# Performance work log

Hardware: AMD Instinct MI355X
Metric: run time of the kernel (lower is better)

## Reference

```python
import jax, jax.numpy as jnp
import numpy as np

B = 32768                 # batch size (number of variants)
NUM_READ_FEATURES = 11
NUM_INFO_FEATURES = 9
PHI_DIMS = [NUM_READ_FEATURES, 64, 64]
OMEGA_DIMS = [NUM_INFO_FEATURES, 64, 64]
RHO_DIMS = [2 * 64 + 64, 128, 64, 1]
CAL_DIMS = [2, 5, 5, 1]


def _counts():
    # deterministic ragged group sizes in [5, 32], mean ~18.5, all nonempty
    return 5 + (np.arange(2 * B) % 28)


def _mlp_params(key, dims, prefix, out):
    for i, (din, dout) in enumerate(zip(dims[:-1], dims[1:])):
        key, k = jax.random.split(key)
        out[f"{prefix}_w{i}"] = (jax.random.normal(k, (din, dout), jnp.float32)
                                  / np.sqrt(din).astype(np.float32))
        out[f"{prefix}_b{i}"] = jnp.zeros((dout,), jnp.float32)
    return key


def _mlp(x, ws_bs):
    # Linear -> ReLU between layers, no activation after the last layer
    n = len(ws_bs) // 2
    for i in range(n):
        x = x @ ws_bs[2 * i] + ws_bs[2 * i + 1]
        if i < n - 1:
            x = jax.nn.relu(x)
    return x


def setup_inputs() -> dict:
    key = jax.random.key(0)
    counts = _counts()
    n_reads = int(counts.sum())  # 1,212,320
    key, k1, k2 = jax.random.split(key, 3)
    out = {
        "reads": jax.random.normal(k1, (n_reads, NUM_READ_FEATURES), jnp.float32),
        "info": jax.random.normal(k2, (B, NUM_INFO_FEATURES), jnp.float32),
        "end_indices": jnp.asarray(np.cumsum(counts), dtype=jnp.int64),
    }
    key = _mlp_params(key, PHI_DIMS, "phi", out)
    key = _mlp_params(key, OMEGA_DIMS, "omega", out)
    key = _mlp_params(key, RHO_DIMS, "rho", out)
    key = _mlp_params(key, CAL_DIMS, "cal", out)
    out["max_logit"] = jnp.asarray(10.0, jnp.float32)
    return out


def reference(reads, info, end_indices,
              phi_w0, phi_b0, phi_w1, phi_b1,
              omega_w0, omega_b0, omega_w1, omega_b1,
              rho_w0, rho_b0, rho_w1, rho_b1, rho_w2, rho_b2,
              cal_w0, cal_b0, cal_w1, cal_b1, cal_w2, cal_b2,
              max_logit):
    n_reads = reads.shape[0]
    num_seg = 2 * B
    # read r belongs to segment j where end_indices[j-1] <= r < end_indices[j]
    seg_ids = jnp.searchsorted(end_indices, jnp.arange(n_reads), side="right")

    phi_reads = jax.nn.sigmoid(_mlp(reads, [phi_w0, phi_b0, phi_w1, phi_b1]))  # [N, 64]
    weights = jnp.ones((n_reads, 1), phi_reads.dtype)  # weight_range == 0
    weighted = weights * phi_reads

    read_sums = jax.ops.segment_sum(weighted, seg_ids, num_segments=num_seg)      # [2B, 64]
    weight_sums = jax.ops.segment_sum(weights, seg_ids, num_segments=num_seg)     # [2B, 1]
    read_means = read_sums / weight_sums
    sq_weight_sums = jax.ops.segment_sum(jnp.square(weights), seg_ids, num_segments=num_seg)
    eff_counts = jnp.square(weight_sums) / sq_weight_sums                          # [2B, 1]

    ref_means, alt_means = read_means[:B], read_means[B:]
    eff_ref, eff_alt = eff_counts[:B], eff_counts[B:]

    omega_info = jax.nn.sigmoid(_mlp(info, [omega_w0, omega_b0, omega_w1, omega_b1]))
    concatenated = jnp.concatenate([ref_means, alt_means, omega_info], axis=1)     # [B, 192]
    logits = jnp.squeeze(_mlp(concatenated, [rho_w0, rho_b0, rho_w1, rho_b1, rho_w2, rho_b2]), -1)

    # Calibration: temperature from sqrt(alt_count), sqrt(ref_count)
    sqrt_counts = jnp.concatenate([jnp.sqrt(eff_alt), jnp.sqrt(eff_ref)], axis=1)  # [B, 2]
    temperatures = jnp.squeeze(_mlp(sqrt_counts, [cal_w0, cal_b0, cal_w1, cal_b1, cal_w2, cal_b2]), -1)
    calibrated = logits * temperatures
    return max_logit * jnp.tanh(calibrated / max_logit)
```

## Files before the change

### kernel.cpp

```cpp
#include <hip/hip_runtime.h>
#include <hip/hip_bf16.h>
#include <math.h>

#define NB 32768
#define NSEG 65536
#define NRF 11
#define NIF 9

typedef __attribute__((ext_vector_type(8))) short bf16x8;
typedef __attribute__((ext_vector_type(4))) float f32x4;

__device__ __forceinline__ short to_bf(float f) {
    __hip_bfloat16 h = __float2bfloat16(f);
    return *reinterpret_cast<short*>(&h);
}
__device__ __forceinline__ float bf2f(short s) {
    __hip_bfloat16 h = *reinterpret_cast<__hip_bfloat16*>(&s);
    return __bfloat162float(h);
}

__global__ __launch_bounds__(256) void k0_prep(
    const float* __restrict__ rw0, const float* __restrict__ rw1,
    const float* __restrict__ pw0, const float* __restrict__ pw1,
    short* __restrict__ w0th, short* __restrict__ w0tl,
    short* __restrict__ w1th, short* __restrict__ w1tl,
    short* __restrict__ p_w0t, short* __restrict__ p_w1t)
{
    const int idx = blockIdx.x * 256 + threadIdx.x;
    if (idx < 192 * 128) {
        const int k = idx >> 7, col = idx & 127;
        const float v = rw0[idx];
        const short hi = to_bf(v);
        const short lo = to_bf(v - bf2f(hi));
        w0th[col * 192 + k] = hi;
        w0tl[col * 192 + k] = lo;
    }
    if (idx < 128 * 64) {
        const int k = idx >> 6, col = idx & 63;
        const float v = rw1[idx];
        const short hi = to_bf(v);
        const short lo = to_bf(v - bf2f(hi));
        w1th[col * 128 + k] = hi;
        w1tl[col * 128 + k] = lo;
    }
    if (idx < 64 * 16) {
        const int col = idx >> 4, k = idx & 15;
        p_w0t[idx] = (k < NRF) ? to_bf(pw0[k * 64 + col]) : (short)0;
    }
    if (idx < 64 * 64) {
        const int col = idx >> 6, k = idx & 63;
        p_w1t[idx] = to_bf(pw1[k * 64 + col]);
    }
}

__global__ __launch_bounds__(256, 4) void k1_phi_mfma3(
    const float* __restrict__ reads,
    const int* __restrict__ endi,
    const short* __restrict__ p_w0t, const short* __restrict__ p_w1t,
    const float* __restrict__ b0, const float* __restrict__ b1,
    float* __restrict__ means)
{
    __shared__ short XA[256][24];
    __shared__ short HB[4][16][64];
    __shared__ int   smeta[9];

    const int tid  = threadIdx.x;
    const int lane = tid & 63;
    const int w    = tid >> 6;
    const int lg   = lane >> 4;
    const int lr   = lane & 15;
    const int k0   = lg * 8;
    const int s0   = blockIdx.x * 8;

    if (tid < 9) {
        const int s = s0 + tid - 1;
        smeta[tid] = (s < 0) ? 0 : endi[s];
    }
    __syncthreads();
    const int rb    = smeta[0];
    const int nrows = smeta[8] - rb;

    const int total = nrows * NRF;
    const float* __restrict__ rbase = reads + (size_t)rb * NRF;
    for (int i = tid; i < total; i += 256) {
        const int row = i / NRF;
        const int col = i - row * NRF;
        XA[row][col] = to_bf(rbase[i]);
    }
    for (int r = tid; r < nrows; r += 256) {
        XA[r][11] = 0;
        *(short4*)&XA[r][12] = (short4){0, 0, 0, 0};
    }
    __syncthreads();

    bf16x8 aW0[4];
#pragma unroll
    for (int nt = 0; nt < 4; ++nt) {
        bf16x8 z = {0, 0, 0, 0, 0, 0, 0, 0};
        if (lg < 2) z = *(const bf16x8*)&p_w0t[(nt * 16 + lr) * 16 + k0];
        aW0[nt] = z;
    }
    bf16x8 bW1[4][2];
#pragma unroll
    for (int nt = 0; nt < 4; ++nt)
#pragma unroll
        for (int ks = 0; ks < 2; ++ks)
            bW1[nt][ks] = *(const bf16x8*)&p_w1t[(nt * 16 + lr) * 64 + ks * 32 + k0];

    f32x4 cbias0[4];
#pragma unroll
    for (int nt = 0; nt < 4; ++nt)
#pragma unroll
        for (int q = 0; q < 4; ++q) cbias0[nt][q] = b0[nt * 16 + 4 * lg + q];
    f32x4 cbias1[4];
#pragma unroll
    for (int nt = 0; nt < 4; ++nt) {
        const float bv = b1[nt * 16 + lr];
#pragma unroll
        for (int q = 0; q < 4; ++q) cbias1[nt][q] = bv;
    }

    for (int q = 0; q < 2; ++q) {
        const int ls  = q * 4 + w;
        const int st  = smeta[ls] - rb;
        const int cnt = smeta[ls + 1] - smeta[ls];
        const int ntl = (cnt + 15) >> 4;
        float segsum[4] = {0.f, 0.f, 0.f, 0.f};

        for (int tt = 0; tt < ntl; ++tt) {
            int lrow = st + tt * 16 + lr;
            lrow = (lrow < nrows) ? lrow : (nrows - 1);
            bf16x8 xb = {0, 0, 0, 0, 0, 0, 0, 0};
            if (lg < 2) xb = *(const bf16x8*)&XA[lrow][k0];

            f32x4 d[4];
#pragma unroll
            for (int nt = 0; nt < 4; ++nt)
                d[nt] = __builtin_amdgcn_mfma_f32_16x16x32_bf16(aW0[nt], xb, cbias0[nt], 0, 0, 0);

#pragma unroll
            for (int nt = 0; nt < 4; ++nt) {
                short4 hp;
                hp.x = to_bf(fmaxf(d[nt][0], 0.f));
                hp.y = to_bf(fmaxf(d[nt][1], 0.f));
                hp.z = to_bf(fmaxf(d[nt][2], 0.f));
                hp.w = to_bf(fmaxf(d[nt][3], 0.f));
                const int blk = (2 * nt + (lg >> 1) + lr) & 7;
                *(short4*)&HB[w][lr][(blk << 3) + ((lg & 1) << 2)] = hp;
            }
            const bf16x8 h0 = *(const bf16x8*)&HB[w][lr][(((lg + lr) & 7) << 3)];
            const bf16x8 h1 = *(const bf16x8*)&HB[w][lr][(((4 + lg + lr) & 7) << 3)];
            f32x4 o[4];
#pragma unroll
            for (int nt = 0; nt < 4; ++nt) {
                f32x4 t = __builtin_amdgcn_mfma_f32_16x16x32_bf16(h0, bW1[nt][0], cbias1[nt], 0, 0, 0);
                o[nt]   = __builtin_amdgcn_mfma_f32_16x16x32_bf16(h1, bW1[nt][1], t, 0, 0, 0);
            }
            const int rowg = tt * 16 + 4 * lg;
#pragma unroll
            for (int nt = 0; nt < 4; ++nt) {
                float s = 0.f;
#pragma unroll
                for (int q2 = 0; q2 < 4; ++q2) {
                    const float p = __builtin_amdgcn_rcpf(1.f + __expf(-o[nt][q2]));
                    s += (rowg + q2 < cnt) ? p : 0.f;
                }
                s += __shfl_xor(s, 16);
                s += __shfl_xor(s, 32);
                segsum[nt] += s;
            }
        }
        if (lg == 0) {
            const float inv = 1.f / (float)cnt;
#pragma unroll
            for (int nt = 0; nt < 4; ++nt)
                means[(size_t)(s0 + ls) * 64 + nt * 16 + lr] = segsum[nt] * inv;
        }
    }
}

__global__ __launch_bounds__(256) void k2_omega(
    const float* __restrict__ info,
    const float* __restrict__ w0, const float* __restrict__ b0,
    const float* __restrict__ w1, const float* __restrict__ b1,
    float* __restrict__ om)
{
    __shared__ float hbuf[4][64];
    const int lane = threadIdx.x & 63;
    const int wid  = threadIdx.x >> 6;
    const int wg   = __builtin_amdgcn_readfirstlane((int)(blockIdx.x * 4 + wid));

    float w0c[NIF];
#pragma unroll
    for (int k = 0; k < NIF; ++k) w0c[k] = w0[k * 64 + lane];
    float w1c[64];
#pragma unroll
    for (int i = 0; i < 64; ++i) w1c[i] = w1[i * 64 + lane];
    const float b0l = b0[lane];
    const float b1l = b1[lane];

    for (int i = 0; i < 8; ++i) {
        const int b = wg * 8 + i;
        const float* __restrict__ x = info + (size_t)b * NIF;
        float h = b0l;
#pragma unroll
        for (int k = 0; k < NIF; ++k) h = fmaf(x[k], w0c[k], h);
        h = fmaxf(h, 0.f);
        hbuf[wid][lane] = h;
        float o = b1l;
        const float4* h4 = (const float4*)(&hbuf[wid][0]);
#pragma unroll
        for (int q = 0; q < 16; ++q) {
            float4 hv = h4[q];
            o = fmaf(hv.x, w1c[4 * q + 0], o);
            o = fmaf(hv.y, w1c[4 * q + 1], o);
            o = fmaf(hv.z, w1c[4 * q + 2], o);
            o = fmaf(hv.w, w1c[4 * q + 3], o);
        }
        om[(size_t)b * 64 + lane] = 1.f / (1.f + __expf(-o));
    }
}

__global__ __launch_bounds__(256) void k3_rho_mfma(
    const float* __restrict__ means, const float* __restrict__ om,
    const int* __restrict__ endi,
    const short* __restrict__ w0th, const short* __restrict__ w0tl,
    const short* __restrict__ w1th, const short* __restrict__ w1tl,
    const float* __restrict__ rb0, const float* __restrict__ rb1,
    const float* __restrict__ rw2, const float* __restrict__ rb2,
    const float* __restrict__ cw0, const float* __restrict__ cb0,
    const float* __restrict__ cw1, const float* __restrict__ cb1,
    const float* __restrict__ cw2, const float* __restrict__ cb2,
    const float* __restrict__ max_logit,
    float* __restrict__ out)
{
    __shared__ __align__(16) char smemA[18432];
    __shared__ __align__(16) char smemB[34816];
    short (*XH)[72]  = (short(*)[72])smemA;
    short (*XL)[72]  = (short(*)[72])(smemA + 9216);
    short (*HH)[136] = (short(*)[136])smemB;
    short (*HL)[136] = (short(*)[136])(smemB + 17408);
    float (*h2T)[68] = (float(*)[68])smemA;

    const int tid  = threadIdx.x;
    const int lane = tid & 63;
    const int w    = tid >> 6;
    const int lg   = lane >> 4;
    const int lr   = lane & 15;
    const int k0   = lg * 8;
    const int b0i  = blockIdx.x * 64;

    const int wbase = w * 32;
    float bias0[2];
#pragma unroll
    for (int nt = 0; nt < 2; ++nt) bias0[nt] = rb0[wbase + nt * 16 + lr];

    f32x4 acc[4][2];
#pragma unroll
    for (int rt = 0; rt < 4; ++rt)
#pragma unroll
        for (int nt = 0; nt < 2; ++nt) acc[rt][nt] = (f32x4){0.f, 0.f, 0.f, 0.f};

    for (int c = 0; c < 3; ++c) {
        const float* __restrict__ src =
            (c == 0) ? means + (size_t)b0i * 64 :
            (c == 1) ? means + (size_t)(NB + b0i) * 64 :
                       om    + (size_t)b0i * 64;
        __syncthreads();
        for (int idx = tid; idx < 64 * 64; idx += 256) {
            const int row = idx >> 6, col = idx & 63;
            const float v = src[(size_t)row * 64 + col];
            const short hi = to_bf(v);
            const short lo = to_bf(v - bf2f(hi));
            XH[row][col] = hi;
            XL[row][col] = lo;
        }
        __syncthreads();

#pragma unroll
        for (int ks = 0; ks < 2; ++ks) {
            const int koff = c * 64 + ks * 32 + k0;
            bf16x8 Bh[2], Bl[2];
#pragma unroll
            for (int nt = 0; nt < 2; ++nt) {
                const int col = wbase + nt * 16 + lr;
                Bh[nt] = *(const bf16x8*)&w0th[(size_t)col * 192 + koff];
                Bl[nt] = *(const bf16x8*)&w0tl[(size_t)col * 192 + koff];
            }
#pragma unroll
            for (int rt = 0; rt < 4; ++rt) {
                const bf16x8 Ah = *(const bf16x8*)&XH[rt * 16 + lr][ks * 32 + k0];
                const bf16x8 Al = *(const bf16x8*)&XL[rt * 16 + lr][ks * 32 + k0];
#pragma unroll
                for (int nt = 0; nt < 2; ++nt) {
                    acc[rt][nt] = __builtin_amdgcn_mfma_f32_16x16x32_bf16(Ah, Bh[nt], acc[rt][nt], 0, 0, 0);
                    acc[rt][nt] = __builtin_amdgcn_mfma_f32_16x16x32_bf16(Al, Bh[nt], acc[rt][nt], 0, 0, 0);
                    acc[rt][nt] = __builtin_amdgcn_mfma_f32_16x16x32_bf16(Ah, Bl[nt], acc[rt][nt], 0, 0, 0);
                }
            }
        }
    }
    __syncthreads();
#pragma unroll
    for (int rt = 0; rt < 4; ++rt)
#pragma unroll
        for (int nt = 0; nt < 2; ++nt)
#pragma unroll
            for (int r = 0; r < 4; ++r) {
                const int row = rt * 16 + 4 * lg + r;
                const int col = wbase + nt * 16 + lr;
                const float v = fmaxf(acc[rt][nt][r] + bias0[nt], 0.f);
                const short hi = to_bf(v);
                HH[row][col] = hi;
                HL[row][col] = to_bf(v - bf2f(hi));
            }
    __syncthreads();

    const int cbase = w * 16;
    const float bias1 = rb1[cbase + lr];
    f32x4 acc2[4];
#pragma unroll
    for (int rt = 0; rt < 4; ++rt) acc2[rt] = (f32x4){0.f, 0.f, 0.f, 0.f};

#pragma unroll
    for (int ks = 0; ks < 4; ++ks) {
        const int koff = ks * 32 + k0;
        const int col  = cbase + lr;
        const bf16x8 Bh = *(const bf16x8*)&w1th[(size_t)col * 128 + koff];
        const bf16x8 Bl = *(const bf16x8*)&w1tl[(size_t)col * 128 + koff];
#pragma unroll
        for (int rt = 0; rt < 4; ++rt) {
            const bf16x8 Ah = *(const bf16x8*)&HH[rt * 16 + lr][koff];
            const bf16x8 Al = *(const bf16x8*)&HL[rt * 16 + lr][koff];
            acc2[rt] = __builtin_amdgcn_mfma_f32_16x16x32_bf16(Ah, Bh, acc2[rt], 0, 0, 0);
            acc2[rt] = __builtin_amdgcn_mfma_f32_16x16x32_bf16(Al, Bh, acc2[rt], 0, 0, 0);
            acc2[rt] = __builtin_amdgcn_mfma_f32_16x16x32_bf16(Ah, Bl, acc2[rt], 0, 0, 0);
        }
    }
#pragma unroll
    for (int rt = 0; rt < 4; ++rt)
#pragma unroll
        for (int r = 0; r < 4; ++r)
            h2T[cbase + lr][rt * 16 + 4 * lg + r] = fmaxf(acc2[rt][r] + bias1, 0.f);
    __syncthreads();

    if (w == 0) {
        const int b = b0i + lane;
        float l0 = rb2[0], l1 = 0.f, l2 = 0.f, l3 = 0.f;
#pragma unroll
        for (int j = 0; j < 16; ++j) {
            l0 = fmaf(h2T[j][lane],      rw2[j],      l0);
            l1 = fmaf(h2T[16 + j][lane], rw2[16 + j], l1);
            l2 = fmaf(h2T[32 + j][lane], rw2[32 + j], l2);
            l3 = fmaf(h2T[48 + j][lane], rw2[48 + j], l3);
        }
        const float logit = (l0 + l1) + (l2 + l3);

        const int er1 = endi[b];
        const int er0 = (b == 0) ? 0 : endi[b - 1];
        const int ea1 = endi[NB + b];
        const int ea0 = endi[NB + b - 1];
        const float x0 = sqrtf((float)(ea1 - ea0));
        const float x1 = sqrtf((float)(er1 - er0));

        float t5[5];
#pragma unroll
        for (int m = 0; m < 5; ++m)
            t5[m] = fmaxf(cb0[m] + x0 * cw0[m] + x1 * cw0[5 + m], 0.f);
        float t5b[5];
#pragma unroll
        for (int m = 0; m < 5; ++m) {
            float v = cb1[m];
#pragma unroll
            for (int i = 0; i < 5; ++i) v = fmaf(t5[i], cw1[i * 5 + m], v);
            t5b[m] = fmaxf(v, 0.f);
        }
        float temp = cb2[0];
#pragma unroll
        for (int m = 0; m < 5; ++m) temp = fmaf(t5b[m], cw2[m], temp);

        const float ml = max_logit[0];
        out[b] = ml * tanhf((logit * temp) / ml);
    }
}

extern "C" void kernel_launch(void* const* d_in, const int* in_sizes, int n_in,
                              void* d_out, int out_size, void* d_ws, size_t ws_size,
                              hipStream_t stream)
{
    const float* reads  = (const float*)d_in[0];
    const float* info   = (const float*)d_in[1];
    const int*   endi   = (const int*)d_in[2];
    const float* phi_w0 = (const float*)d_in[3];
    const float* phi_b0 = (const float*)d_in[4];
    const float* phi_w1 = (const float*)d_in[5];
    const float* phi_b1 = (const float*)d_in[6];
    const float* om_w0  = (const float*)d_in[7];
    const float* om_b0  = (const float*)d_in[8];
    const float* om_w1  = (const float*)d_in[9];
    const float* om_b1  = (const float*)d_in[10];
    const float* rw0    = (const float*)d_in[11];
    const float* rb0    = (const float*)d_in[12];
    const float* rw1    = (const float*)d_in[13];
    const float* rb1    = (const float*)d_in[14];
    const float* rw2    = (const float*)d_in[15];
    const float* rb2    = (const float*)d_in[16];
    const float* cw0    = (const float*)d_in[17];
    const float* cb0    = (const float*)d_in[18];
    const float* cw1    = (const float*)d_in[19];
    const float* cb1    = (const float*)d_in[20];
    const float* cw2    = (const float*)d_in[21];
    const float* cb2    = (const float*)d_in[22];
    const float* mlog   = (const float*)d_in[23];

    char* ws = (char*)d_ws;
    float* means = (float*)ws;
    float* om    = (float*)(ws + 16777216);
    short* w0th  = (short*)(ws + 25165824);
    short* w0tl  = (short*)(ws + 25165824 + 49152);
    short* w1th  = (short*)(ws + 25165824 + 98304);
    short* w1tl  = (short*)(ws + 25165824 + 114688);
    short* p_w0t = (short*)(ws + 25165824 + 131072);
    short* p_w1t = (short*)(ws + 25165824 + 133120);
    float* out   = (float*)d_out;

    hipLaunchKernelGGL(k0_prep, dim3(96), dim3(256), 0, stream,
                       rw0, rw1, phi_w0, phi_w1,
                       w0th, w0tl, w1th, w1tl, p_w0t, p_w1t);
    hipLaunchKernelGGL(k1_phi_mfma3, dim3(8192), dim3(256), 0, stream,
                       reads, endi, p_w0t, p_w1t, phi_b0, phi_b1, means);
    hipLaunchKernelGGL(k2_omega, dim3(1024), dim3(256), 0, stream,
                       info, om_w0, om_b0, om_w1, om_b1, om);
    hipLaunchKernelGGL(k3_rho_mfma, dim3(512), dim3(256), 0, stream,
                       means, om, endi, w0th, w0tl, w1th, w1tl,
                       rb0, rb1, rw2, rb2,
                       cw0, cb0, cw1, cb1, cw2, cb2, mlog, out);
}
```

Measured before the change: 102.4 us.

## Tile packed rows across segments and accumulate via LDS atomics

Instead of each wave processing two segments with per-segment padded 16-row tiles, the block's eight segments' rows are packed contiguously and split into 16-row tiles distributed round-robin over waves. Each 4-row lane group finds its segment by comparing against boundaries and splits its sum between at most two segments, accumulating with shared-memory float atomics. This removes the padding waste from ragged segment sizes and evens out load across waves. The cost is LDS atomic traffic, extra zero padding setup, and the assumption that segments are at least four rows long.

```diff
diff --git a/kernel.cpp b/kernel.cpp
--- a/kernel.cpp
+++ b/kernel.cpp
@@ -53,7 +53,7 @@
     }
 }
 
-__global__ __launch_bounds__(256, 4) void k1_phi_mfma3(
+__global__ __launch_bounds__(256, 4) void k1_phi_mfma4(
     const float* __restrict__ reads,
     const int* __restrict__ endi,
     const short* __restrict__ p_w0t, const short* __restrict__ p_w1t,
@@ -62,6 +62,8 @@
 {
     __shared__ short XA[256][24];
     __shared__ short HB[4][16][64];
+    __shared__ float SS[10][68];
+    __shared__ int   SB[10];
     __shared__ int   smeta[9];
 
     const int tid  = threadIdx.x;
@@ -77,8 +79,13 @@
         smeta[tid] = (s < 0) ? 0 : endi[s];
     }
     __syncthreads();
-    const int rb    = smeta[0];
-    const int nrows = smeta[8] - rb;
+    const int rb     = smeta[0];
+    const int nrows  = smeta[8] - rb;
+    const int ntiles = (nrows + 15) >> 4;
+    const int nprows = ntiles << 4;
+
+    if (tid < 10) SB[tid] = (tid == 9) ? 0x7fffffff : (smeta[tid] - rb);
+    for (int i = tid; i < 10 * 68; i += 256) ((float*)SS)[i] = 0.f;
 
     const int total = nrows * NRF;
     const float* __restrict__ rbase = reads + (size_t)rb * NRF;
@@ -87,9 +94,16 @@
         const int col = i - row * NRF;
         XA[row][col] = to_bf(rbase[i]);
     }
-    for (int r = tid; r < nrows; r += 256) {
-        XA[r][11] = 0;
-        *(short4*)&XA[r][12] = (short4){0, 0, 0, 0};
+    for (int r = tid; r < nprows; r += 256) {
+        if (r < nrows) {
+            XA[r][11] = 0;
+            *(short4*)&XA[r][12] = (short4){0, 0, 0, 0};
+        } else {
+            *(short4*)&XA[r][0]  = (short4){0, 0, 0, 0};
+            *(short4*)&XA[r][4]  = (short4){0, 0, 0, 0};
+            *(short4*)&XA[r][8]  = (short4){0, 0, 0, 0};
+            *(short4*)&XA[r][12] = (short4){0, 0, 0, 0};
+        }
     }
     __syncthreads();
 
@@ -119,63 +133,77 @@
 #pragma unroll
         for (int q = 0; q < 4; ++q) cbias1[nt][q] = bv;
     }
-
-    for (int q = 0; q < 2; ++q) {
-        const int ls  = q * 4 + w;
-        const int st  = smeta[ls] - rb;
-        const int cnt = smeta[ls + 1] - smeta[ls];
-        const int ntl = (cnt + 15) >> 4;
-        float segsum[4] = {0.f, 0.f, 0.f, 0.f};
-
-        for (int tt = 0; tt < ntl; ++tt) {
-            int lrow = st + tt * 16 + lr;
-            lrow = (lrow < nrows) ? lrow : (nrows - 1);
-            bf16x8 xb = {0, 0, 0, 0, 0, 0, 0, 0};
-            if (lg < 2) xb = *(const bf16x8*)&XA[lrow][k0];
-
-            f32x4 d[4];
-#pragma unroll
-            for (int nt = 0; nt < 4; ++nt)
-                d[nt] = __builtin_amdgcn_mfma_f32_16x16x32_bf16(aW0[nt], xb, cbias0[nt], 0, 0, 0);
-
-#pragma unroll
-            for (int nt = 0; nt < 4; ++nt) {
-                short4 hp;
-                hp.x = to_bf(fmaxf(d[nt][0], 0.f));
-                hp.y = to_bf(fmaxf(d[nt][1], 0.f));
-                hp.z = to_bf(fmaxf(d[nt][2], 0.f));
-                hp.w = to_bf(fmaxf(d[nt][3], 0.f));
-                const int blk = (2 * nt + (lg >> 1) + lr) & 7;
-                *(short4*)&HB[w][lr][(blk << 3) + ((lg & 1) << 2)] = hp;
-            }
-            const bf16x8 h0 = *(const bf16x8*)&HB[w][lr][(((lg + lr) & 7) << 3)];
-            const bf16x8 h1 = *(const bf16x8*)&HB[w][lr][(((4 + lg + lr) & 7) << 3)];
-            f32x4 o[4];
-#pragma unroll
-            for (int nt = 0; nt < 4; ++nt) {
-                f32x4 t = __builtin_amdgcn_mfma_f32_16x16x32_bf16(h0, bW1[nt][0], cbias1[nt], 0, 0, 0);
-                o[nt]   = __builtin_amdgcn_mfma_f32_16x16x32_bf16(h1, bW1[nt][1], t, 0, 0, 0);
-            }
-            const int rowg = tt * 16 + 4 * lg;
-#pragma unroll
-            for (int nt = 0; nt < 4; ++nt) {
-                float s = 0.f;
-#pragma unroll
-                for (int q2 = 0; q2 < 4; ++q2) {
-                    const float p = __builtin_amdgcn_rcpf(1.f + __expf(-o[nt][q2]));
-                    s += (rowg + q2 < cnt) ? p : 0.f;
-                }
-                s += __shfl_xor(s, 16);
-                s += __shfl_xor(s, 32);
-                segsum[nt] += s;
-            }
-        }
-        if (lg == 0) {
-            const float inv = 1.f / (float)cnt;
-#pragma unroll
-            for (int nt = 0; nt < 4; ++nt)
-                means[(size_t)(s0 + ls) * 64 + nt * 16 + lr] = segsum[nt] * inv;
-        }
+    int smv[8];
+#pragma unroll
+    for (int i = 0; i < 8; ++i) smv[i] = SB[i + 1];
+
+    for (int t = w; t < ntiles; t += 4) {
+        const int R  = t << 4;
+        const int r0 = R + 4 * lg;
+
+        bf16x8 xb = {0, 0, 0, 0, 0, 0, 0, 0};
+        if (lg < 2) xb = *(const bf16x8*)&XA[R + lr][k0];
+
+        f32x4 d[4];
+#pragma unroll
+        for (int nt = 0; nt < 4; ++nt)
+            d[nt] = __builtin_amdgcn_mfma_f32_16x16x32_bf16(aW0[nt], xb, cbias0[nt], 0, 0, 0);
+
+#pragma unroll
+        for (int nt = 0; nt < 4; ++nt) {
+            short4 hp;
+            hp.x = to_bf(fmaxf(d[nt][0], 0.f));
+            hp.y = to_bf(fmaxf(d[nt][1], 0.f));
+            hp.z = to_bf(fmaxf(d[nt][2], 0.f));
+            hp.w = to_bf(fmaxf(d[nt][3], 0.f));
+            const int blk = (2 * nt + (lg >> 1) + lr) & 7;
+            *(short4*)&HB[w][lr][(blk << 3) + ((lg & 1) << 2)] = hp;
+        }
+        const bf16x8 h0 = *(const bf16x8*)&HB[w][lr][(((lg + lr) & 7) << 3)];
+        const bf16x8 h1 = *(const bf16x8*)&HB[w][lr][(((4 + lg + lr) & 7) << 3)];
+        f32x4 o[4];
+#pragma unroll
+        for (int nt = 0; nt < 4; ++nt) {
+            f32x4 tt = __builtin_amdgcn_mfma_f32_16x16x32_bf16(h0, bW1[nt][0], cbias1[nt], 0, 0, 0);
+            o[nt]    = __builtin_amdgcn_mfma_f32_16x16x32_bf16(h1, bW1[nt][1], tt, 0, 0, 0);
+        }
+
+        float p[4][4];
+#pragma unroll
+        for (int nt = 0; nt < 4; ++nt)
+#pragma unroll
+            for (int q2 = 0; q2 < 4; ++q2)
+                p[nt][q2] = __builtin_amdgcn_rcpf(1.f + __expf(-o[nt][q2]));
+
+        int sa = 0;
+#pragma unroll
+        for (int i = 0; i < 8; ++i) sa += (r0 >= smv[i]) ? 1 : 0;
+        const int ea = SB[sa + 1];
+
+        const float m1 = (r0 + 1 < ea) ? 1.f : 0.f;
+        const float m2 = (r0 + 2 < ea) ? 1.f : 0.f;
+        const float m3 = (r0 + 3 < ea) ? 1.f : 0.f;
+        const float n1 = 1.f - m1, n2 = 1.f - m2, n3 = 1.f - m3;
+
+#pragma unroll
+        for (int nt = 0; nt < 4; ++nt) {
+            float lo = p[nt][0];
+            lo = fmaf(p[nt][1], m1, lo);
+            lo = fmaf(p[nt][2], m2, lo);
+            lo = fmaf(p[nt][3], m3, lo);
+            float hi = p[nt][1] * n1;
+            hi = fmaf(p[nt][2], n2, hi);
+            hi = fmaf(p[nt][3], n3, hi);
+            atomicAdd(&SS[sa][nt * 16 + lr], lo);
+            atomicAdd(&SS[sa + 1][nt * 16 + lr], hi);
+        }
+    }
+    __syncthreads();
+
+    for (int i = tid; i < 512; i += 256) {
+        const int s = i >> 6, c = i & 63;
+        const int cnt = SB[s + 1] - SB[s];
+        means[(size_t)(s0 + s) * 64 + c] = SS[s][c] / (float)cnt;
     }
 }
 
@@ -427,7 +455,7 @@
     hipLaunchKernelGGL(k0_prep, dim3(96), dim3(256), 0, stream,
                        rw0, rw1, phi_w0, phi_w1,
                        w0th, w0tl, w1th, w1tl, p_w0t, p_w1t);
-    hipLaunchKernelGGL(k1_phi_mfma3, dim3(8192), dim3(256), 0, stream,
+    hipLaunchKernelGGL(k1_phi_mfma4, dim3(8192), dim3(256), 0, stream,
                        reads, endi, p_w0t, p_w1t, phi_b0, phi_b1, means);
     hipLaunchKernelGGL(k2_omega, dim3(1024), dim3(256), 0, stream,
                        info, om_w0, om_b0, om_w1, om_b1, om);
```

Result: slower. 278.3 us (+171.7%).
